# Optimization experiments

Hardware: AMD Instinct MI355X
Metric: run time of the kernel (lower is better)

## Reference

```python
import jax, jax.numpy as jnp
import numpy as np
from jax import lax

B, S, H, W = 8, 8, 256, 256  # batch, split_num, crop_size, crop_size


def _sn(w, seed):
    # spectral norm, 1 power iteration, u/v detached (torch spectral_norm semantics)
    o = w.shape[0]
    m = w.reshape(o, -1)
    u = jnp.asarray(np.random.RandomState(seed).randn(o).astype(np.float32))
    u = u / (jnp.linalg.norm(u) + 1e-12)
    v = m.T @ u
    v = v / (jnp.linalg.norm(v) + 1e-12)
    u2 = m @ v
    u2 = u2 / (jnp.linalg.norm(u2) + 1e-12)
    u2 = lax.stop_gradient(u2)
    v = lax.stop_gradient(v)
    sigma = u2 @ (m @ v)
    return w / sigma


def _conv(x, w, stride, groups):
    return lax.conv_general_dilated(x, w, (stride, stride), ((1, 1), (1, 1)),
                                    feature_group_count=groups,
                                    dimension_numbers=('NCHW', 'OIHW', 'NCHW'))


def _inorm(x):
    # InstanceNorm2d(affine=False, eps=1e-5)
    m = x.mean((2, 3), keepdims=True)
    v = ((x - m) ** 2).mean((2, 3), keepdims=True)
    return (x - m) * lax.rsqrt(v + 1e-5)


def _lrelu(x):
    return jnp.where(x >= 0, x, 0.2 * x)


def _crop_resize(img, mask):
    # img [3,H,W], mask [H,W]: mask, bbox of nonzero support, nearest-resize crop to (H,W)
    seg = img * mask
    c = seg.sum(0)
    col = c.sum(0)   # y_seg, per-column sums [W]
    row = c.sum(1)   # x_seg, per-row sums [H]
    cnz = col != 0
    rnz = row != 0
    ok = jnp.any(cnz) & jnp.any(rnz)
    y0 = jnp.argmax(cnz)
    y1 = W - 1 - jnp.argmax(cnz[::-1])
    x0 = jnp.argmax(rnz)
    x1 = H - 1 - jnp.argmax(rnz[::-1])
    h = x1 - x0 + 1
    w = y1 - y0 + 1
    # torch F.interpolate nearest: src = floor(dst * in / out)
    r = x0 + (jnp.arange(H) * h) // H
    cc = y0 + (jnp.arange(W) * w) // W
    resized = seg[:, r[:, None], cc[None, :]]
    return jnp.where(ok, resized, seg)


def _trans_img(real_image, semantic):
    f = jax.vmap(lambda img, masks: jax.vmap(lambda m: _crop_resize(img, m))(masks))
    imgs = f(real_image, semantic)            # [B,S,3,H,W]
    return imgs.reshape(B, S * 3, H, W)


def _forward(real_image, input_semantic, w1, w2, w3, w4, w5, w6, gw1, gb1, gw2, gb2):
    images = _trans_img(real_image, input_semantic)
    a = _lrelu
    x = _inorm(_conv(images, _sn(w1, 1), 2, S))          # [B,64,128,128]
    x = _inorm(_conv(a(x), _sn(w2, 2), 2, S))            # [B,128,64,64]
    out_8 = _inorm(_conv(a(x), _sn(w3, 3), 2, S))        # [B,256,32,32]
    out_16 = _inorm(_conv(a(out_8), _sn(w4, 4), 2, S))   # [B,512,16,16]
    out_32 = _inorm(_conv(a(out_16), _sn(w5, 5), 2, S))  # [B,1024,8,8]
    x = a(_inorm(_conv(a(out_32), _sn(w6, 6), 1, S)))    # [B,2048,8,8]
    x_1 = a(_conv(a(out_16), gw1, 1, 1) + gb1[None, :, None, None])  # [B,2048,16,16]
    x_2 = a(_conv(a(out_8), gw2, 1, 1) + gb2[None, :, None, None])   # [B,2048,32,32]
    return x, x_1, x_2, images


def setup_inputs() -> dict:
    key = jax.random.key(0)
    ks = jax.random.split(key, 12)
    real_image = jax.random.normal(ks[0], (B, 3, H, W), jnp.float32)
    input_semantic = jax.random.randint(ks[1], (B, S, H, W), 0, 2).astype(jnp.float32)
    def cw(k, o, i, kk=3):
        return jax.random.normal(k, (o, i, kk, kk), jnp.float32) * 0.05
    return {
        'real_image': real_image,
        'input_semantic': input_semantic,
        'w1': cw(ks[2], 64, 3),
        'w2': cw(ks[3], 128, 8),
        'w3': cw(ks[4], 256, 16),
        'w4': cw(ks[5], 512, 32),
        'w5': cw(ks[6], 1024, 64),
        'w6': cw(ks[7], 2048, 128),
        'gw1': cw(ks[8], 2048, 512, 1),
        'gb1': jnp.zeros((2048,), jnp.float32),
        'gw2': cw(ks[9], 2048, 256, 1),
        'gb2': jnp.zeros((2048,), jnp.float32),
    }


def reference(real_image, input_semantic, w1, w2, w3, w4, w5, w6, gw1, gb1, gw2, gb2):
    return _forward(real_image, input_semantic, w1, w2, w3, w4, w5, w6, gw1, gb1, gw2, gb2)
```

## Files before the change

kernel.cpp:

```cpp
#include <hip/hip_runtime.h>
#include <math.h>

#define WS_OFF_U     0
#define WS_OFF_T     4096
#define WS_OFF_TN    6400
#define WS_OFF_S2    6408
#define WS_OFF_BBOX  6416
#define WS_OFF_W     8192
#define WS_OFF_C     3152896
#define WS_OFF_D     5250048

#define OUT_X    0
#define OUT_X1   1048576
#define OUT_X2   6356992
#define OUT_IMG  25296896

struct Ptr6 { const float* p[6]; };

typedef short s16x8 __attribute__((ext_vector_type(8)));
typedef float f32x4 __attribute__((ext_vector_type(4)));
typedef unsigned int u32x4 __attribute__((ext_vector_type(4)));

#define MT_UP 0x80000000u
#define MT_LO 0x7fffffffu

__global__ __launch_bounds__(256) void gen_u_par(float* ws){
  const int os[6]   = {64,128,256,512,1024,2048};
  const int uoff[6] = {0,64,192,448,960,1984};
  int l = blockIdx.x;
  int n = os[l];
  int tid = threadIdx.x;

  __shared__ unsigned mt[624];
  __shared__ unsigned draws[8192];
  __shared__ float px[2048], py[2048];
  __shared__ unsigned char accf[2048];
  __shared__ int scan[256];

  if (tid == 0){
    unsigned seed = (unsigned)(l + 1);
    for (int i = 0; i < 624; i++){
      mt[i] = seed;
      seed = 1812433253u * (seed ^ (seed >> 30)) + (unsigned)(i + 1);
    }
  }
  __syncthreads();

  int need = 4 * n;
  int twists = (need + 623) / 624;
  for (int t = 0; t < twists; t++){
    unsigned yA = 0, vA = 0;
    if (tid < 227){ yA = (mt[tid] & MT_UP) | (mt[tid+1] & MT_LO); vA = mt[tid+397]; }
    __syncthreads();
    if (tid < 227){ mt[tid] = vA ^ (yA >> 1) ^ ((yA & 1u) ? 0x9908b0dfu : 0u); }
    __syncthreads();
    unsigned yB = 0, vB = 0; int iB = 227 + tid;
    if (tid < 227){ yB = (mt[iB] & MT_UP) | (mt[iB+1] & MT_LO); vB = mt[iB-227]; }
    __syncthreads();
    if (tid < 227){ mt[iB] = vB ^ (yB >> 1) ^ ((yB & 1u) ? 0x9908b0dfu : 0u); }
    __syncthreads();
    unsigned yC = 0, vC = 0; int iC = 454 + tid;
    if (tid < 169){ yC = (mt[iC] & MT_UP) | (mt[iC+1] & MT_LO); vC = mt[iC-227]; }
    __syncthreads();
    if (tid < 169){ mt[iC] = vC ^ (yC >> 1) ^ ((yC & 1u) ? 0x9908b0dfu : 0u); }
    __syncthreads();
    if (tid == 0){
      unsigned y = (mt[623] & MT_UP) | (mt[0] & MT_LO);
      mt[623] = mt[396] ^ (y >> 1) ^ ((y & 1u) ? 0x9908b0dfu : 0u);
    }
    __syncthreads();
    for (int i = tid; i < 624; i += 256){
      int pos = t * 624 + i;
      if (pos < need){
        unsigned y = mt[i];
        y ^= y >> 11; y ^= (y << 7) & 0x9d2c5680u; y ^= (y << 15) & 0xefc60000u; y ^= y >> 18;
        draws[pos] = y;
      }
    }
    __syncthreads();
  }

  int A = (n + 255) / 256;
  int local = 0;
  for (int a = 0; a < A; a++){
    int k = tid * A + a;
    if (k < n){
      double u1 = ((draws[4*k]   >> 5) * 67108864.0 + (draws[4*k+1] >> 6)) / 9007199254740992.0;
      double u2 = ((draws[4*k+2] >> 5) * 67108864.0 + (draws[4*k+3] >> 6)) / 9007199254740992.0;
      double x1 = 2.0*u1 - 1.0, x2 = 2.0*u2 - 1.0;
      double r2 = x1*x1 + x2*x2;
      int ok = (r2 < 1.0 && r2 != 0.0);
      accf[k] = (unsigned char)ok;
      if (ok){
        double f = sqrt(-2.0 * log(r2) / r2);
        px[k] = (float)(f * x2);
        py[k] = (float)(f * x1);
      }
      local += ok;
    }
  }
  scan[tid] = local;
  __syncthreads();
  if (tid == 0){
    int run = 0;
    for (int i = 0; i < 256; i++){ int c = scan[i]; scan[i] = run; run += c; }
  }
  __syncthreads();
  int j = scan[tid];
  float* u = ws + WS_OFF_U + uoff[l];
  for (int a = 0; a < A; a++){
    int k = tid * A + a;
    if (k < n && accf[k]){
      if (2*j + 1 < n){ u[2*j] = px[k]; u[2*j+1] = py[k]; }
      j++;
    }
  }
}

__global__ __launch_bounds__(256) void sn_t_kernel(Ptr6 wp, float* ws){
  const int cols[6] = {27,72,144,288,576,1152};
  const int uoff[6] = {0,64,192,448,960,1984};
  const int toff[6] = {0,27,99,243,531,1107};
  const int cstart[7] = {0,4,12,28,60,124,252};
  int b = blockIdx.x;
  int l = 0; while (l < 5 && b >= cstart[l+1]) l++;
  int chunk = b - cstart[l];
  int r0 = chunk * 16;
  int C = cols[l];
  const float* m = wp.p[l];
  const float* u = ws + WS_OFF_U + uoff[l];
  float* t = ws + WS_OFF_T + toff[l];
  __shared__ float us[16];
  if (threadIdx.x < 16) us[threadIdx.x] = u[r0 + threadIdx.x];
  __syncthreads();
  for (int j = threadIdx.x; j < C; j += 256){
    float acc = 0.f;
    #pragma unroll
    for (int r = 0; r < 16; r++) acc += m[(size_t)(r0 + r) * C + j] * us[r];
    atomicAdd(&t[j], acc);
  }
}

__global__ void sn_tn_kernel(float* ws){
  const int cols[6] = {27,72,144,288,576,1152};
  const int toff[6] = {0,27,99,243,531,1107};
  int l = blockIdx.x;
  const float* t = ws + WS_OFF_T + toff[l];
  float s = 0.f;
  for (int j = threadIdx.x; j < cols[l]; j += 256){ float v = t[j]; s += v*v; }
  __shared__ float sb[4];
  int lane = threadIdx.x & 63, wid = threadIdx.x >> 6;
  for (int o = 32; o; o >>= 1) s += __shfl_down(s, o, 64);
  if (lane == 0) sb[wid] = s;
  __syncthreads();
  if (threadIdx.x == 0) ws[WS_OFF_TN + l] = sb[0] + sb[1] + sb[2] + sb[3];
}

__global__ __launch_bounds__(256) void sn_z_kernel(Ptr6 wp, float* ws){
  const int cols[6] = {27,72,144,288,576,1152};
  const int toff[6] = {0,27,99,243,531,1107};
  const int rstart[7] = {0,64,192,448,960,1984,4032};
  __shared__ float part[6];
  if (threadIdx.x < 6) part[threadIdx.x] = 0.f;
  __syncthreads();
  int gr = blockIdx.x * 4 + (threadIdx.x >> 6);
  int lane = threadIdx.x & 63;
  if (gr < 4032){
    int l = 0; while (l < 5 && gr >= rstart[l+1]) l++;
    int row = gr - rstart[l];
    int C = cols[l];
    const float* m = wp.p[l] + (size_t)row * C;
    const float* t = ws + WS_OFF_T + toff[l];
    float acc = 0.f;
    for (int c = lane; c < C; c += 64) acc += m[c] * t[c];
    for (int o = 32; o; o >>= 1) acc += __shfl_down(acc, o, 64);
    if (lane == 0) atomicAdd(&part[l], acc * acc);
  }
  __syncthreads();
  if (threadIdx.x < 6 && part[threadIdx.x] != 0.f)
    atomicAdd(&ws[WS_OFF_S2 + threadIdx.x], part[threadIdx.x]);
}

__global__ void wscale_kernel(const float* __restrict__ src, float* __restrict__ dst,
                              int n, const float* __restrict__ tn, const float* __restrict__ s2){
  int i = blockIdx.x * 256 + threadIdx.x;
  if (i >= n) return;
  float inv = sqrtf(tn[0] / s2[0]);
  dst[i] = src[i] * inv;
}

__global__ __launch_bounds__(256) void bbox_stage1(const float* __restrict__ img,
                                                   const float* __restrict__ sem,
                                                   int* __restrict__ colpart,
                                                   int* __restrict__ rowflag){
  int chunk = blockIdx.x;
  int s = blockIdx.y;
  int b = blockIdx.z;
  int w = threadIdx.x;
  int h0 = chunk * 32;
  const float* i0 = img + (size_t)(b*3 + 0) * 65536;
  const float* i1 = i0 + 65536;
  const float* i2 = i1 + 65536;
  const float* mk = sem + (size_t)(b*8 + s) * 65536;
  __shared__ int rflags[32];
  if (w < 32) rflags[w] = 0;
  __syncthreads();
  int lane = w & 63;
  int myflag = 0;
  #pragma unroll 4
  for (int r = 0; r < 32; r++){
    int off = (h0 + r)*256 + w;
    float v = (i0[off] + i1[off] + i2[off]) * mk[off];
    int nz = (v != 0.f);
    myflag |= nz;
    unsigned long long bal = __ballot(nz);
    if (lane == 0 && bal) rflags[r] = 1;
  }
  __syncthreads();
  int bs = b*8 + s;
  colpart[(bs*8 + chunk)*256 + w] = myflag;
  if (w < 32) rowflag[bs*256 + h0 + w] = rflags[w];
}

__global__ __launch_bounds__(256) void bbox_stage2(const int* __restrict__ colpart,
                                                   const int* __restrict__ rowflag,
                                                   int* __restrict__ bbox){
  int bs = blockIdx.x;
  int w = threadIdx.x;
  int colnz = 0;
  #pragma unroll
  for (int c = 0; c < 8; c++) colnz |= colpart[(bs*8 + c)*256 + w];
  int rownz = rowflag[bs*256 + w];
  __shared__ int red[256];
  red[w] = colnz ? w : 256; __syncthreads();
  for (int st = 128; st; st >>= 1){ if (w < st) red[w] = min(red[w], red[w+st]); __syncthreads(); }
  int y0 = red[0]; __syncthreads();
  red[w] = colnz ? w : -1; __syncthreads();
  for (int st = 128; st; st >>= 1){ if (w < st) red[w] = max(red[w], red[w+st]); __syncthreads(); }
  int y1 = red[0]; __syncthreads();
  red[w] = rownz ? w : 256; __syncthreads();
  for (int st = 128; st; st >>= 1){ if (w < st) red[w] = min(red[w], red[w+st]); __syncthreads(); }
  int x0 = red[0]; __syncthreads();
  red[w] = rownz ? w : -1; __syncthreads();
  for (int st = 128; st; st >>= 1){ if (w < st) red[w] = max(red[w], red[w+st]); __syncthreads(); }
  int x1 = red[0];
  if (w == 0){
    int ok = (y0 < 256) && (x0 < 256);
    int base = bs * 4;
    bbox[base+0] = ok ? x0 : 0;
    bbox[base+1] = ok ? (x1 - x0 + 1) : 256;
    bbox[base+2] = ok ? y0 : 0;
    bbox[base+3] = ok ? (y1 - y0 + 1) : 256;
  }
}

__global__ void transimg_kernel(const float* __restrict__ img, const float* __restrict__ sem,
                                const int* __restrict__ bbox, float* __restrict__ out){
  int idx = blockIdx.x * 256 + threadIdx.x;
  int j = idx & 255;
  int i = (idx >> 8) & 255;
  int c = idx >> 16;
  int b = c / 24, ch24 = c % 24;
  int s = ch24 / 3, ch = ch24 % 3;
  const int* bb = bbox + (b*8 + s) * 4;
  int ri = bb[0] + ((i * bb[1]) >> 8);
  int cj = bb[2] + ((j * bb[3]) >> 8);
  float m = sem[((size_t)(b*8 + s) * 256 + ri) * 256 + cj];
  float v = img[((size_t)(b*3 + ch) * 256 + ri) * 256 + cj];
  out[idx] = v * m;
}

template<int CIN_G, int CIN_CHUNK, int COUT_G, int OCC, int RELU_IN>
__global__ __launch_bounds__(256) void conv3x3_tile(const float* __restrict__ in,
                                                    const float* __restrict__ wt,
                                                    float* __restrict__ out,
                                                    int Hin, int Hout){
  constexpr int TIH = 65, TIW = 65, RS = 66;
  constexpr int NOC = COUT_G / OCC;
  constexpr int NSTAGE = CIN_G / CIN_CHUNK;
  __shared__ float xs[CIN_CHUNK][TIH][RS];
  __shared__ float wsh[OCC][CIN_CHUNK*9];
  int tid = threadIdx.x;
  int g = blockIdx.y, b = blockIdx.z;
  int ocChunk = blockIdx.x % NOC;
  int tileId  = blockIdx.x / NOC;
  int tilesX = Hout >> 5;
  int tileX = tileId % tilesX, tileY = tileId / tilesX;
  int oh0 = tileY*32, ow0 = tileX*32;
  int ih0 = oh0*2 - 1, iw0 = ow0*2 - 1;
  int sx = tid & 15, sy = tid >> 4;
  const int Cin_tot = CIN_G*8;

  float acc[OCC][2][2];
  #pragma unroll
  for (int o = 0; o < OCC; o++)
    #pragma unroll
    for (int i2 = 0; i2 < 2; i2++)
      #pragma unroll
      for (int j2 = 0; j2 < 2; j2++) acc[o][i2][j2] = 0.f;

  for (int st = 0; st < NSTAGE; st++){
    int icb = st*CIN_CHUNK;
    for (int i = tid; i < CIN_CHUNK*TIH*TIW; i += 256){
      int ic = i / (TIH*TIW);
      int rem = i - ic*(TIH*TIW);
      int r = rem / TIW, c = rem - r*TIW;
      int ih = ih0 + r, iw = iw0 + c;
      float v = 0.f;
      if ((unsigned)ih < (unsigned)Hin && (unsigned)iw < (unsigned)Hin){
        v = in[((size_t)(b*Cin_tot + g*CIN_G + icb + ic)*Hin + ih)*Hin + iw];
        if (RELU_IN) v = (v >= 0.f) ? v : 0.2f*v;
      }
      xs[ic][r][c] = v;
    }
    for (int i = tid; i < OCC*CIN_CHUNK*9; i += 256){
      int o = i / (CIN_CHUNK*9);
      int rr = i - o*(CIN_CHUNK*9);
      int ic = rr / 9, tap = rr - ic*9;
      wsh[o][rr] = wt[((size_t)(g*COUT_G + ocChunk*OCC + o)*CIN_G + icb + ic)*9 + tap];
    }
    __syncthreads();
    #pragma unroll
    for (int ic = 0; ic < CIN_CHUNK; ic++){
      #pragma unroll
      for (int kh = 0; kh < 3; kh++){
        #pragma unroll
        for (int kw = 0; kw < 3; kw++){
          float wv[OCC];
          #pragma unroll
          for (int o = 0; o < OCC; o++) wv[o] = wsh[o][ic*9 + kh*3 + kw];
          #pragma unroll
          for (int i2 = 0; i2 < 2; i2++){
            #pragma unroll
            for (int j2 = 0; j2 < 2; j2++){
              float x = xs[ic][2*(sy + 16*i2) + kh][2*(sx + 16*j2) + kw];
              #pragma unroll
              for (int o = 0; o < OCC; o++) acc[o][i2][j2] += wv[o]*x;
            }
          }
        }
      }
    }
    if (st + 1 < NSTAGE) __syncthreads();
  }

  #pragma unroll
  for (int o = 0; o < OCC; o++){
    int oc = g*COUT_G + ocChunk*OCC + o;
    #pragma unroll
    for (int i2 = 0; i2 < 2; i2++)
      #pragma unroll
      for (int j2 = 0; j2 < 2; j2++){
        int oh = oh0 + sy + 16*i2, ow = ow0 + sx + 16*j2;
        out[((size_t)(b*COUT_G*8 + oc)*Hout + oh)*Hout + ow] = acc[o][i2][j2];
      }
  }
}

template<int STRIDE, int CIN_G, int COUT_G, int HSH>
__global__ __launch_bounds__(256) void conv3x3_gemm(const float* __restrict__ in,
                                                    const float* __restrict__ wt,
                                                    float* __restrict__ out,
                                                    int Hin){
  constexpr int K = CIN_G*9;
  const int Hout = 1 << HSH;
  int z = blockIdx.z; int b = z >> 3, g = z & 7;
  int n0 = blockIdx.x * 64, oc0 = blockIdx.y * 64;
  __shared__ float Ws[16][68];
  __shared__ float Xs[16][68];
  int tid = threadIdx.x;
  int tx = tid & 15, ty = tid >> 4;
  int pixl = tid & 63;
  int kkb = (tid >> 6) << 2;
  float acc[4][4];
  #pragma unroll
  for (int i = 0; i < 4; i++)
    #pragma unroll
    for (int j = 0; j < 4; j++) acc[i][j] = 0.f;

  for (int k0 = 0; k0 < K; k0 += 16){
    #pragma unroll
    for (int r = 0; r < 4; r++){
      int oc_l = (tid >> 4) + 16*r;
      int kk = tid & 15;
      Ws[kk][oc_l] = wt[((size_t)(g*COUT_G + oc0 + oc_l))*K + k0 + kk];
    }
    #pragma unroll
    for (int r = 0; r < 4; r++){
      int kk = kkb + r;
      int k = k0 + kk;
      int ic = k / 9, tap = k - ic*9;
      int dh = tap / 3, dw = tap - dh*3;
      int n = n0 + pixl;
      int oh = n >> HSH, ow = n & (Hout - 1);
      int ih = oh*STRIDE - 1 + dh, iw = ow*STRIDE - 1 + dw;
      float v = 0.f;
      if ((unsigned)ih < (unsigned)Hin && (unsigned)iw < (unsigned)Hin){
        v = in[((size_t)(b*CIN_G*8 + g*CIN_G + ic)*Hin + ih)*Hin + iw];
        v = (v >= 0.f) ? v : 0.2f*v;
      }
      Xs[kk][pixl] = v;
    }
    __syncthreads();
    #pragma unroll
    for (int kk = 0; kk < 16; kk++){
      float4 wv = *(const float4*)&Ws[kk][ty*4];
      float4 xv = *(const float4*)&Xs[kk][tx*4];
      acc[0][0] += wv.x*xv.x; acc[0][1] += wv.x*xv.y; acc[0][2] += wv.x*xv.z; acc[0][3] += wv.x*xv.w;
      acc[1][0] += wv.y*xv.x; acc[1][1] += wv.y*xv.y; acc[1][2] += wv.y*xv.z; acc[1][3] += wv.y*xv.w;
      acc[2][0] += wv.z*xv.x; acc[2][1] += wv.z*xv.y; acc[2][2] += wv.z*xv.z; acc[2][3] += wv.z*xv.w;
      acc[3][0] += wv.w*xv.x; acc[3][1] += wv.w*xv.y; acc[3][2] += wv.w*xv.z; acc[3][3] += wv.w*xv.w;
    }
    __syncthreads();
  }

  #pragma unroll
  for (int i = 0; i < 4; i++){
    int oc = g*COUT_G + oc0 + ty*4 + i;
    #pragma unroll
    for (int j = 0; j < 4; j++){
      int n = n0 + tx*4 + j;
      int oh = n >> HSH, ow = n & (Hout - 1);
      out[((size_t)(b*COUT_G*8 + oc)*Hout + oh)*Hout + ow] = acc[i][j];
    }
  }
}

__global__ void inorm_kernel(const float* __restrict__ in, float* __restrict__ out,
                             int N, int relu_out){
  int bc = blockIdx.x;
  const float* p = in + (size_t)bc * N;
  float* q = out + (size_t)bc * N;
  float s = 0.f, ss = 0.f;
  for (int i = threadIdx.x; i < N; i += blockDim.x){ float x = p[i]; s += x; ss += x*x; }
  __shared__ float sb[8];
  int lane = threadIdx.x & 63, wid = threadIdx.x >> 6;
  for (int o = 32; o; o >>= 1){ s += __shfl_down(s, o, 64); ss += __shfl_down(ss, o, 64); }
  if (lane == 0){ sb[wid] = s; sb[4 + wid] = ss; }
  __syncthreads();
  if (threadIdx.x == 0){
    int nw = blockDim.x >> 6;
    float S = 0.f, SS = 0.f;
    for (int i = 0; i < nw; i++){ S += sb[i]; SS += sb[4+i]; }
    float mean = S / N;
    float var = SS / N - mean*mean;
    sb[0] = mean;
    sb[4] = rsqrtf(var + 1e-5f);
  }
  __syncthreads();
  float mean = sb[0], r = sb[4];
  for (int i = threadIdx.x; i < N; i += blockDim.x){
    float y = (p[i] - mean) * r;
    if (relu_out) y = (y >= 0.f) ? y : 0.2f*y;
    q[i] = y;
  }
}

template<int P>
__global__ void inorm_sum(const float* __restrict__ in, float* __restrict__ out,
                          int N, size_t pstride, int relu_out){
  int bc = blockIdx.x;
  const float* p = in + (size_t)bc * N;
  float* q = out + (size_t)bc * N;
  float s = 0.f, ss = 0.f;
  for (int i = threadIdx.x; i < N; i += blockDim.x){
    float x = 0.f;
    #pragma unroll
    for (int pp = 0; pp < P; pp++) x += p[(size_t)pp*pstride + i];
    q[i] = x;
    s += x; ss += x*x;
  }
  __shared__ float sb[8];
  int lane = threadIdx.x & 63, wid = threadIdx.x >> 6;
  for (int o = 32; o; o >>= 1){ s += __shfl_down(s, o, 64); ss += __shfl_down(ss, o, 64); }
  if (lane == 0){ sb[wid] = s; sb[4 + wid] = ss; }
  __syncthreads();
  if (threadIdx.x == 0){
    int nw = blockDim.x >> 6;
    float S = 0.f, SS = 0.f;
    for (int i = 0; i < nw; i++){ S += sb[i]; SS += sb[4+i]; }
    float mean = S / N;
    float var = SS / N - mean*mean;
    sb[0] = mean;
    sb[4] = rsqrtf(var + 1e-5f);
  }
  __syncthreads();
  float mean = sb[0], r = sb[4];
  for (int i = threadIdx.x; i < N; i += blockDim.x){
    float y = (q[i] - mean) * r;
    if (relu_out) y = (y >= 0.f) ? y : 0.2f*y;
    q[i] = y;
  }
}

__device__ __forceinline__ void split_bf16(float v, unsigned short& h, unsigned short& l){
  unsigned u = __float_as_uint(v);
  unsigned r = (u + 0x7FFFu + ((u >> 16) & 1u)) >> 16;
  h = (unsigned short)r;
  float hf = __uint_as_float(r << 16);
  float lo = v - hf;
  unsigned u2 = __float_as_uint(lo);
  unsigned r2 = (u2 + 0x7FFFu + ((u2 >> 16) & 1u)) >> 16;
  l = (unsigned short)r2;
}

template<int C, int HW>
__global__ __launch_bounds__(256) void cvt_x_kernel(const float* __restrict__ src,
                                                    unsigned short* __restrict__ dst){
  __shared__ float tile[64][65];
  int b = blockIdx.z;
  int c0 = blockIdx.y * 64, p0 = blockIdx.x * 64;
  const float* sp = src + ((size_t)b*C + c0)*HW + p0;
  for (int i = threadIdx.x; i < 64*64; i += 256){
    int ch = i >> 6, px = i & 63;
    float v = sp[(size_t)ch*HW + px];
    tile[ch][px] = (v >= 0.f) ? v : 0.2f*v;
  }
  __syncthreads();
  unsigned short* dp = dst + ((size_t)b*HW + p0)*(3*C) + c0;
  for (int i = threadIdx.x; i < 64*64; i += 256){
    int px = i >> 6, ch = i & 63;
    float v = tile[ch][px];
    unsigned short h, l; split_bf16(v, h, l);
    unsigned short* row = dp + (size_t)px*(3*C);
    row[ch] = h; row[C + ch] = l; row[2*C + ch] = h;
  }
}

template<int C>
__global__ __launch_bounds__(256) void cvt_w_kernel(const float* __restrict__ wt,
                                                    unsigned short* __restrict__ dst){
  int i = blockIdx.x * 256 + threadIdx.x;
  int oc = i / C, k = i & (C - 1);
  float v = wt[i];
  unsigned short h, l; split_bf16(v, h, l);
  unsigned short* row = dst + (size_t)oc * 3 * C;
  row[k] = h; row[C + k] = h; row[2*C + k] = l;
}

template<int K>
__global__ __launch_bounds__(256) void cvt_w_g(const float* __restrict__ wt,
                                               unsigned short* __restrict__ dst, int total){
  int i = blockIdx.x * 256 + threadIdx.x;
  if (i >= total) return;
  int oc = i / K, k = i - oc*K;
  float v = wt[i];
  unsigned short h, l; split_bf16(v, h, l);
  unsigned short* row = dst + (size_t)oc * 3 * K;
  row[k] = h; row[K + k] = h; row[2*K + k] = l;
}

template<int K, int K3PAD>
__global__ __launch_bounds__(256) void cvt_w_pad(const float* __restrict__ wt,
                                                 unsigned short* __restrict__ dst, int total){
  int i = blockIdx.x * 256 + threadIdx.x;
  if (i >= total) return;
  int oc = i / K3PAD, kk = i - oc*K3PAD;
  unsigned short o = 0;
  if (kk < 3*K){
    int which = kk / K, k = kk - which*K;
    float v = wt[(size_t)oc*K + k];
    unsigned short h, l; split_bf16(v, h, l);
    o = (which == 2) ? l : h;
  }
  dst[i] = o;
}

template<int CIN_G, int Hin, int STRIDE>
__global__ __launch_bounds__(256) void cvt_im2col(const float* __restrict__ in,
                                                  unsigned short* __restrict__ dst){
  constexpr int K = CIN_G*9;
  constexpr int K3 = 3*K;
  int g = blockIdx.x, b = blockIdx.y, pc = blockIdx.z;
  const float* src = in + (size_t)(b*CIN_G*8 + g*CIN_G)*Hin*Hin;
  unsigned short* drow = dst + ((size_t)g*512 + b*64 + pc*16)*K3;
  for (int idx = threadIdx.x; idx < 16*K; idx += 256){
    int pixl = idx / K, k = idx - pixl*K;
    int ic = k / 9, tap = k - ic*9;
    int dh = tap / 3, dw = tap - dh*3;
    int gp = pc*16 + pixl;
    int oh = gp >> 3, ow = gp & 7;
    int ih = oh*STRIDE - 1 + dh, iw = ow*STRIDE - 1 + dw;
    float v = 0.f;
    if ((unsigned)ih < (unsigned)Hin && (unsigned)iw < (unsigned)Hin){
      v = src[((size_t)ic*Hin + ih)*Hin + iw];
      v = (v >= 0.f) ? v : 0.2f*v;
    }
    unsigned short h, l; split_bf16(v, h, l);
    unsigned short* row = drow + (size_t)pixl*K3;
    row[k] = h; row[K + k] = l; row[2*K + k] = h;
  }
}

template<int CIN_G, int Hin, int HOSH, int STRIDE, int K3PAD, int NB>
__global__ __launch_bounds__(256) void cvt_im2col_g(const float* __restrict__ in,
                                                    unsigned short* __restrict__ dst, int b0){
  constexpr int K = CIN_G*9;
  constexpr int Hout = 1 << HOSH;
  constexpr int HW = Hout*Hout;
  int g = blockIdx.x, bl = blockIdx.y, pc = blockIdx.z;
  int b = b0 + bl;
  const float* src = in + (size_t)(b*CIN_G*8 + g*CIN_G)*Hin*Hin;
  unsigned short* drow = dst + ((size_t)g*(NB*HW) + (size_t)bl*HW + pc*64)*K3PAD;
  for (int idx = threadIdx.x; idx < 64*K; idx += 256){
    int pixl = idx / K, k = idx - pixl*K;
    int ic = k / 9, tap = k - ic*9;
    int dh = tap / 3, dw = tap - dh*3;
    int gp = pc*64 + pixl;
    int oh = gp >> HOSH, ow = gp & (Hout - 1);
    int ih = oh*STRIDE - 1 + dh, iw = ow*STRIDE - 1 + dw;
    float v = 0.f;
    if ((unsigned)ih < (unsigned)Hin && (unsigned)iw < (unsigned)Hin){
      v = src[((size_t)ic*Hin + ih)*Hin + iw];
      v = (v >= 0.f) ? v : 0.2f*v;
    }
    unsigned short h, l; split_bf16(v, h, l);
    unsigned short* row = drow + (size_t)pixl*K3PAD;
    row[k] = h; row[K + k] = l; row[2*K + k] = h;
  }
  for (int idx = threadIdx.x; idx < 64*(K3PAD - 3*K); idx += 256){
    int pixl = idx / (K3PAD - 3*K), k = idx - pixl*(K3PAD - 3*K);
    drow[(size_t)pixl*K3PAD + 3*K + k] = 0;
  }
}

template<int K3, int HW, int H>
__global__ __launch_bounds__(256) void conv1x1_mfma(const unsigned short* __restrict__ XT,
                                                    const unsigned short* __restrict__ WT,
                                                    const float* __restrict__ bias,
                                                    float* __restrict__ out){
  constexpr int Wp = H + 2;
  constexpr int NKT = K3 / 64;
  __shared__ unsigned short As[8*128*8];
  __shared__ unsigned short Bs[8*128*8];
  int tid = threadIdx.x;
  int b = blockIdx.z;
  int oc0 = blockIdx.y * 128;
  int px0 = blockIdx.x * 128;
  int lane = tid & 63;
  int wv = tid >> 6;
  int wy = wv >> 1, wx = wv & 1;

  int srow = tid >> 3;
  int sc8  = tid & 7;
  const unsigned short* Ag = WT + (size_t)(oc0 + srow)*K3 + sc8*8;
  const unsigned short* Bg = XT + ((size_t)b*HW + px0 + srow)*K3 + sc8*8;

  f32x4 acc[4][4];
  #pragma unroll
  for (int i = 0; i < 4; i++)
    #pragma unroll
    for (int j = 0; j < 4; j++) acc[i][j] = (f32x4){0.f,0.f,0.f,0.f};

  for (int kt = 0; kt < NKT; kt++){
    int k0 = kt * 64;
    #pragma unroll
    for (int q = 0; q < 4; q++){
      u32x4 av = *(const u32x4*)(Ag + (size_t)(32*q)*K3 + k0);
      u32x4 bv = *(const u32x4*)(Bg + (size_t)(32*q)*K3 + k0);
      int rr = srow + 32*q;
      *(u32x4*)&As[(sc8*128 + (rr ^ sc8))*8] = av;
      *(u32x4*)&Bs[(sc8*128 + (rr ^ sc8))*8] = bv;
    }
    __syncthreads();
    #pragma unroll
    for (int s = 0; s < 2; s++){
      int cb = s*4 + (lane >> 4);
      s16x8 af[4], bfr[4];
      #pragma unroll
      for (int mt = 0; mt < 4; mt++){
        int row = wy*64 + mt*16 + (lane & 15);
        af[mt] = *(const s16x8*)&As[(cb*128 + (row ^ cb))*8];
      }
      #pragma unroll
      for (int nt = 0; nt < 4; nt++){
        int row = wx*64 + nt*16 + (lane & 15);
        bfr[nt] = *(const s16x8*)&Bs[(cb*128 + (row ^ cb))*8];
      }
      #pragma unroll
      for (int mt = 0; mt < 4; mt++)
        #pragma unroll
        for (int nt = 0; nt < 4; nt++)
          acc[mt][nt] = __builtin_amdgcn_mfma_f32_16x16x32_bf16(af[mt], bfr[nt], acc[mt][nt], 0, 0, 0);
    }
    __syncthreads();
  }

  #pragma unroll
  for (int mt = 0; mt < 4; mt++){
    #pragma unroll
    for (int r = 0; r < 4; r++){
      int oc = oc0 + wy*64 + mt*16 + (lane >> 4)*4 + r;
      float bv2 = bias[oc];
      float* ob = out + ((size_t)b*2048 + oc)*Wp*Wp;
      #pragma unroll
      for (int nt = 0; nt < 4; nt++){
        int pix = px0 + wx*64 + nt*16 + (lane & 15);
        int ph = pix / H, pw2 = pix % H;
        float v = acc[mt][nt][r] + bv2;
        v = (v >= 0.f) ? v : 0.2f*v;
        ob[(size_t)(ph + 1)*Wp + pw2 + 1] = v;
      }
    }
  }
}

template<int K3, int COUT_G, int CTOT, int KSPLIT>
__global__ __launch_bounds__(256) void grouped_mfma(const unsigned short* __restrict__ XT,
                                                    const unsigned short* __restrict__ WT,
                                                    float* __restrict__ out, size_t pstride){
  constexpr int NKT = K3 / 64;
  constexpr int SPK = NKT / KSPLIT;
  __shared__ unsigned short As[8*128*8];
  __shared__ unsigned short Bs[8*128*8];
  int tid = threadIdx.x;
  int oc0 = blockIdx.y * 128;
  int g = oc0 / COUT_G;
  int px0 = blockIdx.x * 128;
  int ks = blockIdx.z;
  out += (size_t)ks * pstride;
  int lane = tid & 63;
  int wv = tid >> 6;
  int wy = wv >> 1, wx = wv & 1;

  int srow = tid >> 3;
  int sc8  = tid & 7;
  const unsigned short* Ag = WT + (size_t)(oc0 + srow)*K3 + sc8*8;
  const unsigned short* Bg = XT + ((size_t)g*512 + px0 + srow)*K3 + sc8*8;

  f32x4 acc[4][4];
  #pragma unroll
  for (int i = 0; i < 4; i++)
    #pragma unroll
    for (int j = 0; j < 4; j++) acc[i][j] = (f32x4){0.f,0.f,0.f,0.f};

  for (int kt = ks*SPK; kt < (ks+1)*SPK; kt++){
    int k0 = kt * 64;
    #pragma unroll
    for (int q = 0; q < 4; q++){
      u32x4 av = *(const u32x4*)(Ag + (size_t)(32*q)*K3 + k0);
      u32x4 bv = *(const u32x4*)(Bg + (size_t)(32*q)*K3 + k0);
      int rr = srow + 32*q;
      *(u32x4*)&As[(sc8*128 + (rr ^ sc8))*8] = av;
      *(u32x4*)&Bs[(sc8*128 + (rr ^ sc8))*8] = bv;
    }
    __syncthreads();
    #pragma unroll
    for (int s = 0; s < 2; s++){
      int cb = s*4 + (lane >> 4);
      s16x8 af[4], bfr[4];
      #pragma unroll
      for (int mt = 0; mt < 4; mt++){
        int row = wy*64 + mt*16 + (lane & 15);
        af[mt] = *(const s16x8*)&As[(cb*128 + (row ^ cb))*8];
      }
      #pragma unroll
      for (int nt = 0; nt < 4; nt++){
        int row = wx*64 + nt*16 + (lane & 15);
        bfr[nt] = *(const s16x8*)&Bs[(cb*128 + (row ^ cb))*8];
      }
      #pragma unroll
      for (int mt = 0; mt < 4; mt++)
        #pragma unroll
        for (int nt = 0; nt < 4; nt++)
          acc[mt][nt] = __builtin_amdgcn_mfma_f32_16x16x32_bf16(af[mt], bfr[nt], acc[mt][nt], 0, 0, 0);
    }
    __syncthreads();
  }

  #pragma unroll
  for (int mt = 0; mt < 4; mt++){
    #pragma unroll
    for (int r = 0; r < 4; r++){
      int oc = oc0 + wy*64 + mt*16 + (lane >> 4)*4 + r;
      #pragma unroll
      for (int nt = 0; nt < 4; nt++){
        int row = px0 + wx*64 + nt*16 + (lane & 15);
        int b = row >> 6, p = row & 63;
        out[((size_t)(b*CTOT + oc))*64 + p] = acc[mt][nt][r];
      }
    }
  }
}

template<int K3PAD, int COUT_G, int CTOT, int HW, int NROWS>
__global__ __launch_bounds__(256) void gconv_mfma(const unsigned short* __restrict__ XT,
                                                  const unsigned short* __restrict__ WT,
                                                  float* __restrict__ out, int b0){
  constexpr int NKT = K3PAD / 64;
  constexpr int MF = COUT_G / 16;
  __shared__ unsigned short As[8*COUT_G*8];
  __shared__ unsigned short Bs[8*128*8];
  int tid = threadIdx.x;
  int g = blockIdx.y;
  int px0 = blockIdx.x * 128;
  int lane = tid & 63;
  int wv = tid >> 6;

  int srow = tid >> 3;
  int sc8  = tid & 7;
  const unsigned short* Ag = WT + (size_t)(g*COUT_G + (srow & (COUT_G-1)))*K3PAD + sc8*8;
  const unsigned short* Bg = XT + ((size_t)g*NROWS + px0 + srow)*K3PAD + sc8*8;

  f32x4 acc[MF][2];
  #pragma unroll
  for (int i = 0; i < MF; i++)
    #pragma unroll
    for (int j = 0; j < 2; j++) acc[i][j] = (f32x4){0.f,0.f,0.f,0.f};

  for (int kt = 0; kt < NKT; kt++){
    int k0 = kt * 64;
    if (srow < COUT_G)
      *(u32x4*)&As[(sc8*COUT_G + (srow ^ sc8))*8] = *(const u32x4*)(Ag + k0);
    #pragma unroll
    for (int q = 0; q < 4; q++){
      int rr = srow + 32*q;
      *(u32x4*)&Bs[(sc8*128 + (rr ^ sc8))*8] = *(const u32x4*)(Bg + (size_t)(32*q)*K3PAD + k0);
    }
    __syncthreads();
    #pragma unroll
    for (int s = 0; s < 2; s++){
      int cb = s*4 + (lane >> 4);
      s16x8 af[MF], bfr[2];
      #pragma unroll
      for (int mt = 0; mt < MF; mt++){
        int row = mt*16 + (lane & 15);
        af[mt] = *(const s16x8*)&As[(cb*COUT_G + (row ^ cb))*8];
      }
      #pragma unroll
      for (int nt = 0; nt < 2; nt++){
        int row = wv*32 + nt*16 + (lane & 15);
        bfr[nt] = *(const s16x8*)&Bs[(cb*128 + (row ^ cb))*8];
      }
      #pragma unroll
      for (int mt = 0; mt < MF; mt++)
        #pragma unroll
        for (int nt = 0; nt < 2; nt++)
          acc[mt][nt] = __builtin_amdgcn_mfma_f32_16x16x32_bf16(af[mt], bfr[nt], acc[mt][nt], 0, 0, 0);
    }
    __syncthreads();
  }

  #pragma unroll
  for (int mt = 0; mt < MF; mt++){
    #pragma unroll
    for (int r = 0; r < 4; r++){
      int oc = g*COUT_G + mt*16 + (lane >> 4)*4 + r;
      #pragma unroll
      for (int nt = 0; nt < 2; nt++){
        int rowg = px0 + wv*32 + nt*16 + (lane & 15);
        int bl = rowg / HW, px = rowg - bl*HW;
        out[((size_t)((b0 + bl)*CTOT + oc))*HW + px] = acc[mt][nt][r];
      }
    }
  }
}

__global__ void border_kernel(const float* __restrict__ bias, float* __restrict__ out, int H){
  int Wp = H + 2, perim = 4*Wp - 4;
  int p = threadIdx.x;
  if (p >= perim) return;
  int oc = blockIdx.y, b = blockIdx.z;
  int ph, pw;
  if (p < Wp){ ph = 0; pw = p; }
  else if (p < 2*Wp){ ph = Wp - 1; pw = p - Wp; }
  else { int q = p - 2*Wp; ph = 1 + (q >> 1); pw = (q & 1) ? (Wp - 1) : 0; }
  float bv = bias[oc];
  bv = (bv >= 0.f) ? bv : 0.2f*bv;
  out[(((size_t)b*2048 + oc)*Wp + ph)*Wp + pw] = bv;
}

extern "C" void kernel_launch(void* const* d_in, const int* in_sizes, int n_in,
                              void* d_out, int out_size, void* d_ws, size_t ws_size,
                              hipStream_t stream){
  const float* img = (const float*)d_in[0];
  const float* sem = (const float*)d_in[1];
  Ptr6 wp;
  for (int l = 0; l < 6; l++) wp.p[l] = (const float*)d_in[2 + l];
  const float* gw1 = (const float*)d_in[8];
  const float* gb1 = (const float*)d_in[9];
  const float* gw2 = (const float*)d_in[10];
  const float* gb2 = (const float*)d_in[11];
  float* out = (float*)d_out;
  float* ws  = (float*)d_ws;

  float* bufA = out + OUT_X2;
  float* bufB = bufA + 8388608;
  float* bufC = ws + WS_OFF_C;
  float* bufD = ws + WS_OFF_D;
  int* bbox = (int*)(ws + WS_OFF_BBOX);
  int* colpart = (int*)(bufB + 8388608);
  int* rowflag = colpart + 64*8*256;

  unsigned short* XT2 = (unsigned short*)(out + OUT_X1);
  unsigned short* W2  = (unsigned short*)(out + OUT_X1 + 3145728);
  unsigned short* XT1 = (unsigned short*)(ws + WS_OFF_W);
  unsigned short* W1  = (unsigned short*)(ws + WS_OFF_W + 1572864);

  unsigned short* XT5 = (unsigned short*)(bufA + 1048576);
  unsigned short* W5s = (unsigned short*)(bufB);
  unsigned short* XT6 = (unsigned short*)(bufA + 1048576);
  unsigned short* W6s = (unsigned short*)(bufB + 1048576);

  unsigned short* X3i = (unsigned short*)bufA;
  unsigned short* W3s = (unsigned short*)(bufB + 8388608);
  float* out3raw = out + OUT_X1;

  unsigned short* X2i = (unsigned short*)bufA;
  unsigned short* W2s = (unsigned short*)(bufB + 8388608 + 57344);
  float* out2raw = out + OUT_X1;

  static const int kWOff[6]  = {0,1728,10944,47808,195264,785088};
  static const int kWSize[6] = {1728,9216,36864,147456,589824,2359296};

  hipMemsetAsync(ws + WS_OFF_T, 0, (WS_OFF_S2 + 8 - WS_OFF_T) * sizeof(float), stream);

  gen_u_par<<<6, 256, 0, stream>>>(ws);
  sn_t_kernel<<<252, 256, 0, stream>>>(wp, ws);
  sn_tn_kernel<<<6, 256, 0, stream>>>(ws);
  sn_z_kernel<<<1008, 256, 0, stream>>>(wp, ws);
  for (int l = 0; l < 6; l++)
    wscale_kernel<<<(kWSize[l]+255)/256, 256, 0, stream>>>(wp.p[l], ws + WS_OFF_W + kWOff[l],
                                                           kWSize[l], ws + WS_OFF_TN + l, ws + WS_OFF_S2 + l);

  bbox_stage1<<<dim3(8,8,8), 256, 0, stream>>>(img, sem, colpart, rowflag);
  bbox_stage2<<<64, 256, 0, stream>>>(colpart, rowflag, bbox);
  transimg_kernel<<<49152, 256, 0, stream>>>(img, sem, bbox, out + OUT_IMG);

  conv3x3_tile<3,3,8,8,0><<<dim3(16,8,8), 256, 0, stream>>>(out + OUT_IMG, ws + WS_OFF_W + kWOff[0],
                                                            bufA, 256, 128);
  inorm_kernel<<<512, 256, 0, stream>>>(bufA, bufB, 16384, 0);

  cvt_w_pad<72,256><<<(128*256+255)/256, 256, 0, stream>>>(ws + WS_OFF_W + kWOff[1], W2s, 128*256);
  for (int s = 0; s < 4; s++){
    cvt_im2col_g<8,128,6,2,256,2><<<dim3(8,2,64), 256, 0, stream>>>(bufB, X2i, 2*s);
    gconv_mfma<256,16,128,4096,8192><<<dim3(64,8), 256, 0, stream>>>(X2i, W2s, out2raw, 2*s);
  }
  inorm_kernel<<<1024, 256, 0, stream>>>(out2raw, bufB, 4096, 0);

  cvt_w_pad<144,448><<<(256*448+255)/256, 256, 0, stream>>>(ws + WS_OFF_W + kWOff[2], W3s, 256*448);
  for (int s = 0; s < 2; s++){
    cvt_im2col_g<16,64,5,2,448,4><<<dim3(8,4,16), 256, 0, stream>>>(bufB, X3i, 4*s);
    gconv_mfma<448,32,256,1024,4096><<<dim3(32,8), 256, 0, stream>>>(X3i, W3s, out3raw, 4*s);
  }
  inorm_kernel<<<2048, 256, 0, stream>>>(out3raw, bufC, 1024, 0);

  conv3x3_gemm<2,32,64,4><<<dim3(4,1,64), 256, 0, stream>>>(bufC, ws + WS_OFF_W + kWOff[3], bufA, 32);
  inorm_kernel<<<4096, 256, 0, stream>>>(bufA, bufD, 256, 0);

  cvt_im2col<64,16,2><<<dim3(8,8,4), 256, 0, stream>>>(bufD, XT5);
  cvt_w_g<576><<<2304, 256, 0, stream>>>(ws + WS_OFF_W + kWOff[4], W5s, 589824);
  grouped_mfma<1728,128,1024,3><<<dim3(4,8,3), 256, 0, stream>>>(XT5, W5s, out + OUT_X1, 524288);
  inorm_sum<3><<<8192, 64, 0, stream>>>(out + OUT_X1, bufB, 64, 524288, 0);

  cvt_im2col<128,8,1><<<dim3(8,8,4), 256, 0, stream>>>(bufB, XT6);
  cvt_w_g<1152><<<9216, 256, 0, stream>>>(ws + WS_OFF_W + kWOff[5], W6s, 2359296);
  grouped_mfma<3456,256,2048,6><<<dim3(4,16,6), 256, 0, stream>>>(XT6, W6s, out, 1048576);
  inorm_sum<6><<<16384, 64, 0, stream>>>(out, out + OUT_X, 64, 1048576, 1);

  cvt_x_kernel<256,1024><<<dim3(16,4,8), 256, 0, stream>>>(bufC, XT2);
  cvt_w_kernel<256><<<2048, 256, 0, stream>>>(gw2, W2);
  cvt_x_kernel<512,256><<<dim3(4,8,8), 256, 0, stream>>>(bufD, XT1);
  cvt_w_kernel<512><<<4096, 256, 0, stream>>>(gw1, W1);

  border_kernel<<<dim3(1,2048,8), 256, 0, stream>>>(gb2, out + OUT_X2, 32);
  conv1x1_mfma<768,1024,32><<<dim3(8,16,8), 256, 0, stream>>>(XT2, W2, gb2, out + OUT_X2);
  border_kernel<<<dim3(1,2048,8), 256, 0, stream>>>(gb1, out + OUT_X1, 16);
  conv1x1_mfma<1536,256,16><<<dim3(2,16,8), 256, 0, stream>>>(XT1, W1, gb1, out + OUT_X1);
}
```

Before: 630.0 us.

## Move layer-4 grouped conv to bf16 MFMA im2col path with split-K partials

Replaces the FP32 shared-memory GEMM used for the fourth 3x3 grouped conv with the bf16 im2col and MFMA gconv kernel. The gconv kernel gains a K-split over blockIdx.z that writes partial sums to separate buffers, which inorm_sum then adds while normalising. Weight tile loading is generalised so it can cover more than 32 output channels per group. The aim is to run this layer on matrix cores and raise block count; in exchange it adds conversion kernels, extra partial-sum traffic and bf16 rounding.

```diff
diff --git a/kernel.cpp b/kernel.cpp
--- a/kernel.cpp
+++ b/kernel.cpp
@@ -357,75 +357,6 @@
   }
 }
 
-template<int STRIDE, int CIN_G, int COUT_G, int HSH>
-__global__ __launch_bounds__(256) void conv3x3_gemm(const float* __restrict__ in,
-                                                    const float* __restrict__ wt,
-                                                    float* __restrict__ out,
-                                                    int Hin){
-  constexpr int K = CIN_G*9;
-  const int Hout = 1 << HSH;
-  int z = blockIdx.z; int b = z >> 3, g = z & 7;
-  int n0 = blockIdx.x * 64, oc0 = blockIdx.y * 64;
-  __shared__ float Ws[16][68];
-  __shared__ float Xs[16][68];
-  int tid = threadIdx.x;
-  int tx = tid & 15, ty = tid >> 4;
-  int pixl = tid & 63;
-  int kkb = (tid >> 6) << 2;
-  float acc[4][4];
-  #pragma unroll
-  for (int i = 0; i < 4; i++)
-    #pragma unroll
-    for (int j = 0; j < 4; j++) acc[i][j] = 0.f;
-
-  for (int k0 = 0; k0 < K; k0 += 16){
-    #pragma unroll
-    for (int r = 0; r < 4; r++){
-      int oc_l = (tid >> 4) + 16*r;
-      int kk = tid & 15;
-      Ws[kk][oc_l] = wt[((size_t)(g*COUT_G + oc0 + oc_l))*K + k0 + kk];
-    }
-    #pragma unroll
-    for (int r = 0; r < 4; r++){
-      int kk = kkb + r;
-      int k = k0 + kk;
-      int ic = k / 9, tap = k - ic*9;
-      int dh = tap / 3, dw = tap - dh*3;
-      int n = n0 + pixl;
-      int oh = n >> HSH, ow = n & (Hout - 1);
-      int ih = oh*STRIDE - 1 + dh, iw = ow*STRIDE - 1 + dw;
-      float v = 0.f;
-      if ((unsigned)ih < (unsigned)Hin && (unsigned)iw < (unsigned)Hin){
-        v = in[((size_t)(b*CIN_G*8 + g*CIN_G + ic)*Hin + ih)*Hin + iw];
-        v = (v >= 0.f) ? v : 0.2f*v;
-      }
-      Xs[kk][pixl] = v;
-    }
-    __syncthreads();
-    #pragma unroll
-    for (int kk = 0; kk < 16; kk++){
-      float4 wv = *(const float4*)&Ws[kk][ty*4];
-      float4 xv = *(const float4*)&Xs[kk][tx*4];
-      acc[0][0] += wv.x*xv.x; acc[0][1] += wv.x*xv.y; acc[0][2] += wv.x*xv.z; acc[0][3] += wv.x*xv.w;
-      acc[1][0] += wv.y*xv.x; acc[1][1] += wv.y*xv.y; acc[1][2] += wv.y*xv.z; acc[1][3] += wv.y*xv.w;
-      acc[2][0] += wv.z*xv.x; acc[2][1] += wv.z*xv.y; acc[2][2] += wv.z*xv.z; acc[2][3] += wv.z*xv.w;
-      acc[3][0] += wv.w*xv.x; acc[3][1] += wv.w*xv.y; acc[3][2] += wv.w*xv.z; acc[3][3] += wv.w*xv.w;
-    }
-    __syncthreads();
-  }
-
-  #pragma unroll
-  for (int i = 0; i < 4; i++){
-    int oc = g*COUT_G + oc0 + ty*4 + i;
-    #pragma unroll
-    for (int j = 0; j < 4; j++){
-      int n = n0 + tx*4 + j;
-      int oh = n >> HSH, ow = n & (Hout - 1);
-      out[((size_t)(b*COUT_G*8 + oc)*Hout + oh)*Hout + ow] = acc[i][j];
-    }
-  }
-}
-
 __global__ void inorm_kernel(const float* __restrict__ in, float* __restrict__ out,
                              int N, int relu_out){
   int bc = blockIdx.x;
@@ -783,24 +714,27 @@
   }
 }
 
-template<int K3PAD, int COUT_G, int CTOT, int HW, int NROWS>
+template<int K3PAD, int COUT_G, int CTOT, int HW, int NROWS, int KSPLIT>
 __global__ __launch_bounds__(256) void gconv_mfma(const unsigned short* __restrict__ XT,
                                                   const unsigned short* __restrict__ WT,
-                                                  float* __restrict__ out, int b0){
+                                                  float* __restrict__ out, int b0, size_t pstride){
   constexpr int NKT = K3PAD / 64;
+  constexpr int SPK = NKT / KSPLIT;
   constexpr int MF = COUT_G / 16;
   __shared__ unsigned short As[8*COUT_G*8];
   __shared__ unsigned short Bs[8*128*8];
   int tid = threadIdx.x;
   int g = blockIdx.y;
   int px0 = blockIdx.x * 128;
+  int ks = blockIdx.z;
+  out += (size_t)ks * pstride;
   int lane = tid & 63;
   int wv = tid >> 6;
 
   int srow = tid >> 3;
   int sc8  = tid & 7;
-  const unsigned short* Ag = WT + (size_t)(g*COUT_G + (srow & (COUT_G-1)))*K3PAD + sc8*8;
-  const unsigned short* Bg = XT + ((size_t)g*NROWS + px0 + srow)*K3PAD + sc8*8;
+  const unsigned short* Agb = WT + (size_t)(g*COUT_G)*K3PAD + sc8*8;
+  const unsigned short* Bg  = XT + ((size_t)g*NROWS + px0 + srow)*K3PAD + sc8*8;
 
   f32x4 acc[MF][2];
   #pragma unroll
@@ -808,10 +742,14 @@
     #pragma unroll
     for (int j = 0; j < 2; j++) acc[i][j] = (f32x4){0.f,0.f,0.f,0.f};
 
-  for (int kt = 0; kt < NKT; kt++){
+  for (int kt = ks*SPK; kt < (ks+1)*SPK; kt++){
     int k0 = kt * 64;
-    if (srow < COUT_G)
-      *(u32x4*)&As[(sc8*COUT_G + (srow ^ sc8))*8] = *(const u32x4*)(Ag + k0);
+    #pragma unroll
+    for (int q = 0; q < (COUT_G + 31)/32; q++){
+      int rr = srow + 32*q;
+      if (rr < COUT_G)
+        *(u32x4*)&As[(sc8*COUT_G + (rr ^ sc8))*8] = *(const u32x4*)(Agb + (size_t)rr*K3PAD + k0);
+    }
     #pragma unroll
     for (int q = 0; q < 4; q++){
       int rr = srow + 32*q;
@@ -902,13 +840,16 @@
   unsigned short* XT6 = (unsigned short*)(bufA + 1048576);
   unsigned short* W6s = (unsigned short*)(bufB + 1048576);
 
+  unsigned short* W3s = (unsigned short*)(bufB + 8388608);
+  unsigned short* W2s = (unsigned short*)(bufB + 8388608 + 57344);
+  unsigned short* W4s = (unsigned short*)(bufB + 8388608 + 73728);
+
+  unsigned short* X2i = (unsigned short*)bufA;
+  float* out2raw = out + OUT_X1;
   unsigned short* X3i = (unsigned short*)bufA;
-  unsigned short* W3s = (unsigned short*)(bufB + 8388608);
   float* out3raw = out + OUT_X1;
-
-  unsigned short* X2i = (unsigned short*)bufA;
-  unsigned short* W2s = (unsigned short*)(bufB + 8388608 + 57344);
-  float* out2raw = out + OUT_X1;
+  unsigned short* X4i = (unsigned short*)bufA;
+  float* out4raw = out + OUT_X1;
 
   static const int kWOff[6]  = {0,1728,10944,47808,195264,785088};
   static const int kWSize[6] = {1728,9216,36864,147456,589824,2359296};
@@ -934,19 +875,21 @@
   cvt_w_pad<72,256><<<(128*256+255)/256, 256, 0, stream>>>(ws + WS_OFF_W + kWOff[1], W2s, 128*256);
   for (int s = 0; s < 4; s++){
     cvt_im2col_g<8,128,6,2,256,2><<<dim3(8,2,64), 256, 0, stream>>>(bufB, X2i, 2*s);
-    gconv_mfma<256,16,128,4096,8192><<<dim3(64,8), 256, 0, stream>>>(X2i, W2s, out2raw, 2*s);
+    gconv_mfma<256,16,128,4096,8192,1><<<dim3(64,8), 256, 0, stream>>>(X2i, W2s, out2raw, 2*s, 0);
   }
   inorm_kernel<<<1024, 256, 0, stream>>>(out2raw, bufB, 4096, 0);
 
   cvt_w_pad<144,448><<<(256*448+255)/256, 256, 0, stream>>>(ws + WS_OFF_W + kWOff[2], W3s, 256*448);
   for (int s = 0; s < 2; s++){
     cvt_im2col_g<16,64,5,2,448,4><<<dim3(8,4,16), 256, 0, stream>>>(bufB, X3i, 4*s);
-    gconv_mfma<448,32,256,1024,4096><<<dim3(32,8), 256, 0, stream>>>(X3i, W3s, out3raw, 4*s);
+    gconv_mfma<448,32,256,1024,4096,1><<<dim3(32,8), 256, 0, stream>>>(X3i, W3s, out3raw, 4*s, 0);
   }
   inorm_kernel<<<2048, 256, 0, stream>>>(out3raw, bufC, 1024, 0);
 
-  conv3x3_gemm<2,32,64,4><<<dim3(4,1,64), 256, 0, stream>>>(bufC, ws + WS_OFF_W + kWOff[3], bufA, 32);
-  inorm_kernel<<<4096, 256, 0, stream>>>(bufA, bufD, 256, 0);
+  cvt_w_pad<288,896><<<(512*896+255)/256, 256, 0, stream>>>(ws + WS_OFF_W + kWOff[3], W4s, 512*896);
+  cvt_im2col_g<32,32,4,2,896,8><<<dim3(8,8,4), 256, 0, stream>>>(bufC, X4i, 0);
+  gconv_mfma<896,64,512,256,2048,2><<<dim3(16,8,2), 256, 0, stream>>>(X4i, W4s, out4raw, 0, 1048576);
+  inorm_sum<2><<<4096, 256, 0, stream>>>(out4raw, bufD, 256, 1048576, 0);
 
   cvt_im2col<64,16,2><<<dim3(8,8,4), 256, 0, stream>>>(bufD, XT5);
   cvt_w_g<576><<<2304, 256, 0, stream>>>(ws + WS_OFF_W + kWOff[4], W5s, 589824);
```

After: 662.1 us. 5.1% more time.
